# Optimization experiments

Hardware: AMD Instinct MI355X
Metric: run time of the kernel (lower is better)

Reference implementation:

```python
import jax, jax.numpy as jnp
import numpy as np

NUM_AREAS = 4
NUM_TICKS = 4
AREA_N = 2048          # neurons per area
N = NUM_AREAS * AREA_N # total neurons = 8192
D_IN = 1024
N_CLASSES = 1024
BATCH = 512
THRESHOLD = 0.05


def setup_inputs() -> dict:
    key = jax.random.key(0)
    ks = jax.random.split(key, 9)
    x = jax.random.normal(ks[0], (BATCH, D_IN), jnp.float32)
    Rw = jax.random.normal(ks[1], (NUM_AREAS, AREA_N, D_IN), jnp.float32) * 0.02
    rb = jax.random.normal(ks[2], (NUM_AREAS, AREA_N), jnp.float32) * 0.02
    W_blocks = jax.random.normal(ks[3], (NUM_AREAS, NUM_AREAS, AREA_N, AREA_N), jnp.float32) * 0.02
    # bias only on diagonal blocks (in_area == out_area), else zeros, as in torch code
    b_full = jax.random.normal(ks[4], (NUM_AREAS, AREA_N), jnp.float32) * 0.02
    b_blocks = jnp.zeros((NUM_AREAS, NUM_AREAS, AREA_N), jnp.float32)
    b_blocks = b_blocks.at[jnp.arange(NUM_AREAS), jnp.arange(NUM_AREAS)].set(b_full)
    # mask init: 0.5 on diagonal blocks, 0.05 off-diagonal
    eye = jnp.eye(NUM_AREAS, dtype=jnp.float32)
    mask = (0.05 + 0.45 * eye)[:, :, None, None] * jnp.ones((NUM_AREAS, NUM_AREAS, AREA_N, AREA_N), jnp.float32)
    Ow = jax.random.normal(ks[5], (N_CLASSES, N), jnp.float32) * 0.02
    Ob = jax.random.normal(ks[6], (N_CLASSES,), jnp.float32) * 0.02
    # KMeans-like neuron partition: random permutation split into equal areas
    area_idx = jax.random.permutation(ks[7], N).reshape(NUM_AREAS, AREA_N).astype(jnp.int64)
    return {"x": x, "Rw": Rw, "rb": rb, "W_blocks": W_blocks, "b_blocks": b_blocks,
            "mask": mask, "Ow": Ow, "Ob": Ob, "area_idx": area_idx}


def reference(x, Rw, rb, W_blocks, b_blocks, mask, Ow, Ob, area_idx):
    # Initial per-area encoding: Z[a] = tanh(x @ Rw[a].T + rb[a]) -> [A, B, n]
    Z = jnp.tanh(jnp.einsum('bd,and->abn', x, Rw) + rb[:, None, :])
    history = [Z]
    # Effective masked weights (clamp mask to [0,1])
    Weff = W_blocks * jnp.clip(mask, 0.0, 1.0)  # [A_out, A_in, n_out, n_in]
    for _ in range(NUM_TICKS):
        # data-dependent skip: connection fires only if mean|Z_in| > threshold
        gate = (jnp.mean(jnp.abs(Z), axis=(1, 2)) > THRESHOLD).astype(Z.dtype)  # [A_in]
        Zg = Z * gate[:, None, None]
        Z_next = jnp.einsum('ibm,oinm->obn', Zg, Weff)
        Z_next = Z_next + jnp.einsum('i,oin->on', gate, b_blocks)[:, None, :]
        Z = jnp.tanh(Z_next)
        history.append(Z)
    B = x.shape[0]
    # Scatter per-area activations back to flat neuron order
    Zperm = jnp.transpose(Z, (1, 0, 2)).reshape(B, N)  # columns ordered as area_idx.reshape(-1)
    Z_flat = jnp.zeros((B, N), x.dtype).at[:, area_idx.reshape(-1)].set(Zperm)
    logits = Z_flat @ Ow.T + Ob
    return logits, jnp.stack(history)  # history: [T+1, A, B, n]
```

## Files before the change

### kernel.cpp

```cpp
#include <hip/hip_runtime.h>
#include <stdint.h>

typedef unsigned short u16;
typedef float floatx4 __attribute__((ext_vector_type(4)));
typedef __bf16 bf16x8 __attribute__((ext_vector_type(8)));
typedef float f32x4v __attribute__((ext_vector_type(4)));
typedef unsigned u32x4v __attribute__((ext_vector_type(4)));

#define NUM_AREAS 4
#define AN 2048
#define NTOT 8192
#define BATCH 512
#define DIN 1024
#define NCLS 1024
#define THRESHOLD 0.05f
#define BAN (BATCH * AN)

__device__ __forceinline__ u16 f2bf(float f) {
    union { float f; unsigned u; } v; v.f = f;
    unsigned r = v.u + 0x7fffu + ((v.u >> 16) & 1u);
    return (u16)(r >> 16);
}

__device__ __forceinline__ void load_lds16(const u16* g, u16* l) {
    __builtin_amdgcn_global_load_lds((const __attribute__((address_space(1))) void*)g,
                                     (__attribute__((address_space(3))) void*)l,
                                     16, 0, 0);
}

__device__ __forceinline__ void gemm_db(const u16* __restrict__ A, int lda,
                                        const u16* __restrict__ Bm, int ldb,
                                        int klen, u16* sA, u16* sB,
                                        floatx4 acc[4][4]) {
    const int tid = threadIdx.x;
    const int t8 = tid * 8;
    const int lane = tid & 63;
    const int quad = lane >> 4;
    const int l15 = lane & 15;
    const int wm = ((tid >> 7) & 1) * 64;
    const int wn = ((tid >> 6) & 1) * 64;
    const int r0 = t8 >> 5;
    const int kk = t8 & 31;
    const int nst = klen >> 5;

    auto stage = [&](int buf, int k0) {
        const int bo = buf << 12;
        load_lds16(A + (size_t)r0 * lda + (k0 + kk), sA + bo + t8);
        load_lds16(Bm + (size_t)r0 * ldb + (k0 + kk), sB + bo + t8);
        load_lds16(A + (size_t)(r0 + 64) * lda + (k0 + kk), sA + bo + 2048 + t8);
        load_lds16(Bm + (size_t)(r0 + 64) * ldb + (k0 + kk), sB + bo + 2048 + t8);
    };

    stage(0, 0);
    __syncthreads();
    int buf = 0;
    for (int t = 0; t < nst; ++t) {
        const int bo = buf << 12;
        bf16x8 av[4], bv[4];
#pragma unroll
        for (int i = 0; i < 4; ++i)
            av[i] = *(const bf16x8*)(sA + bo + (wm + i * 16 + l15) * 32 + quad * 8);
#pragma unroll
        for (int i = 0; i < 4; ++i)
            bv[i] = *(const bf16x8*)(sB + bo + (wn + i * 16 + l15) * 32 + quad * 8);
        if (t + 1 < nst) stage(buf ^ 1, (t + 1) << 5);
#pragma unroll
        for (int mt = 0; mt < 4; ++mt)
#pragma unroll
            for (int nt = 0; nt < 4; ++nt)
                acc[mt][nt] = __builtin_amdgcn_mfma_f32_16x16x32_bf16(av[mt], bv[nt], acc[mt][nt], 0, 0, 0);
        __syncthreads();
        buf ^= 1;
    }
}

__global__ void k_init(const float* __restrict__ Ob, float* __restrict__ out,
                       float* __restrict__ gacc) {
    const int i = blockIdx.x * 256 + threadIdx.x;
    if (i < BATCH * NCLS) out[i] = Ob[i & (NCLS - 1)];
    if (i < 32) gacc[i] = 0.f;
}

__global__ void k_cvt(const float* __restrict__ src, u16* __restrict__ dst, int n8) {
    const int i = blockIdx.x * 256 + threadIdx.x;
    if (i >= n8) return;
    const float4 x0 = ((const float4*)src)[2 * i];
    const float4 x1 = ((const float4*)src)[2 * i + 1];
    uint4 o;
    o.x = (unsigned)f2bf(x0.x) | ((unsigned)f2bf(x0.y) << 16);
    o.y = (unsigned)f2bf(x0.z) | ((unsigned)f2bf(x0.w) << 16);
    o.z = (unsigned)f2bf(x1.x) | ((unsigned)f2bf(x1.y) << 16);
    o.w = (unsigned)f2bf(x1.z) | ((unsigned)f2bf(x1.w) << 16);
    ((uint4*)dst)[i] = o;
}

__global__ void k_weff(const float* __restrict__ W, const float* __restrict__ mask,
                       u16* __restrict__ dst) {
    const int i = blockIdx.x * 256 + threadIdx.x;
    const f32x4v* wp = (const f32x4v*)W + (size_t)4 * i;
    const f32x4v* mp = (const f32x4v*)mask + (size_t)4 * i;
    f32x4v w0 = wp[0], w1 = wp[1], w2 = wp[2], w3 = wp[3];
    f32x4v m0 = mp[0], m1 = mp[1], m2 = mp[2], m3 = mp[3];
    asm volatile("" :: "v"(w0), "v"(w1), "v"(w2), "v"(w3),
                       "v"(m0), "v"(m1), "v"(m2), "v"(m3));
    #define CL(m) fminf(fmaxf((m), 0.f), 1.f)
    #define PK(wa, ma, wb, mb) ((unsigned)f2bf((wa) * CL(ma)) | ((unsigned)f2bf((wb) * CL(mb)) << 16))
    u32x4v o0, o1;
    o0[0] = PK(w0[0], m0[0], w0[1], m0[1]);
    o0[1] = PK(w0[2], m0[2], w0[3], m0[3]);
    o0[2] = PK(w1[0], m1[0], w1[1], m1[1]);
    o0[3] = PK(w1[2], m1[2], w1[3], m1[3]);
    o1[0] = PK(w2[0], m2[0], w2[1], m2[1]);
    o1[1] = PK(w2[2], m2[2], w2[3], m2[3]);
    o1[2] = PK(w3[0], m3[0], w3[1], m3[1]);
    o1[3] = PK(w3[2], m3[2], w3[3], m3[3]);
    #undef PK
    #undef CL
    u32x4v* dp = (u32x4v*)dst + (size_t)2 * i;
    dp[0] = o0;
    dp[1] = o1;
}

__global__ void k_enc(const u16* __restrict__ xbf, const u16* __restrict__ rwbf,
                      const float* __restrict__ rb, float* __restrict__ hist0,
                      u16* __restrict__ z0, float* __restrict__ gacc) {
    __shared__ __align__(16) u16 smemA[8192];
    __shared__ __align__(16) u16 smemB[8192];
    __shared__ float red[4];
    floatx4 acc[4][4] = {};
    const int mb = blockIdx.y, nb = blockIdx.x;
    gemm_db(xbf + (size_t)mb * 128 * DIN, DIN,
            rwbf + (size_t)nb * 128 * DIN, DIN, DIN, smemA, smemB, acc);
    const int tid = threadIdx.x, lane = tid & 63, quad = lane >> 4, l15 = lane & 15;
    const int wm = ((tid >> 7) & 1) * 64, wn = ((tid >> 6) & 1) * 64;
    const int cbase = nb * 128;
    const int area = cbase >> 11;
    float asum = 0.f;
#pragma unroll
    for (int nt = 0; nt < 4; ++nt) {
        const int col = cbase + wn + nt * 16 + l15;
        const int n = col & (AN - 1);
        const float bias = rb[col];
#pragma unroll
        for (int mt = 0; mt < 4; ++mt) {
#pragma unroll
            for (int r = 0; r < 4; ++r) {
                const int row = mb * 128 + wm + mt * 16 + quad * 4 + r;
                const float z = tanhf(acc[mt][nt][r] + bias);
                asum += fabsf(z);
                const size_t idx = (size_t)area * BAN + (size_t)row * AN + n;
                hist0[idx] = z;
                z0[idx] = f2bf(z);
            }
        }
    }
    for (int off = 32; off > 0; off >>= 1) asum += __shfl_down(asum, off, 64);
    if (lane == 0) red[tid >> 6] = asum;
    __syncthreads();
    if (tid == 0) atomicAdd(&gacc[area], red[0] + red[1] + red[2] + red[3]);
}

__global__ void k_tick_mm(const u16* __restrict__ zprev, const u16* __restrict__ weff,
                          const float* __restrict__ gin, float* __restrict__ zacc) {
    __shared__ __align__(16) u16 smemA[8192];
    __shared__ __align__(16) u16 smemB[8192];
    const int nb = blockIdx.x, mb = blockIdx.y, i = blockIdx.z;
    const float thr = THRESHOLD * (float)BAN;
    if (!(gin[i] > thr)) return;
    floatx4 acc[4][4] = {};
    const int cbase = nb * 128;
    const int o = cbase >> 11;
    const int nbase = cbase & (AN - 1);
    gemm_db(zprev + (size_t)i * BAN + (size_t)mb * 128 * AN, AN,
            weff + ((size_t)(o * 4 + i) * AN + nbase) * AN, AN, AN,
            smemA, smemB, acc);
    float* __restrict__ dst = zacc + ((size_t)i * 4 + o) * BAN;
    const int tid = threadIdx.x, lane = tid & 63, quad = lane >> 4, l15 = lane & 15;
    const int wm = ((tid >> 7) & 1) * 64, wn = ((tid >> 6) & 1) * 64;
#pragma unroll
    for (int nt = 0; nt < 4; ++nt) {
        const int n = nbase + wn + nt * 16 + l15;
#pragma unroll
        for (int mt = 0; mt < 4; ++mt) {
#pragma unroll
            for (int r = 0; r < 4; ++r) {
                const int row = mb * 128 + wm + mt * 16 + quad * 4 + r;
                dst[(size_t)row * AN + n] = acc[mt][nt][r];
            }
        }
    }
}

__global__ void k_tick_ep(const float* __restrict__ zacc, const float* __restrict__ bblk,
                          const float* __restrict__ gin, float* __restrict__ hist,
                          u16* __restrict__ zcur, float* __restrict__ gout) {
    __shared__ float red[4];
    const int tid = threadIdx.x;
    const int t8 = (blockIdx.x * 256 + tid) * 8;
    const int o = t8 >> 20;
    const int n = t8 & (AN - 1);
    const int io = t8 & (BAN - 1);
    const float thr = THRESHOLD * (float)BAN;
    float s[8] = {0.f, 0.f, 0.f, 0.f, 0.f, 0.f, 0.f, 0.f};
#pragma unroll
    for (int i = 0; i < 4; ++i) {
        if (!(gin[i] > thr)) continue;
        const float4* p = (const float4*)(zacc + ((size_t)i * 4 + o) * BAN + io);
        const float4 x0 = p[0], x1 = p[1];
        const float4* bb = (const float4*)(bblk + (size_t)(o * 4 + i) * AN + n);
        const float4 b0 = bb[0], b1 = bb[1];
        s[0] += x0.x + b0.x; s[1] += x0.y + b0.y; s[2] += x0.z + b0.z; s[3] += x0.w + b0.w;
        s[4] += x1.x + b1.x; s[5] += x1.y + b1.y; s[6] += x1.z + b1.z; s[7] += x1.w + b1.w;
    }
    float4 h0, h1;
    uint4 zb;
    const float z0 = tanhf(s[0]), z1 = tanhf(s[1]), z2 = tanhf(s[2]), z3 = tanhf(s[3]);
    const float z4 = tanhf(s[4]), z5 = tanhf(s[5]), z6 = tanhf(s[6]), z7 = tanhf(s[7]);
    float asum = fabsf(z0) + fabsf(z1) + fabsf(z2) + fabsf(z3)
               + fabsf(z4) + fabsf(z5) + fabsf(z6) + fabsf(z7);
    h0.x = z0; h0.y = z1; h0.z = z2; h0.w = z3;
    h1.x = z4; h1.y = z5; h1.z = z6; h1.w = z7;
    zb.x = (unsigned)f2bf(z0) | ((unsigned)f2bf(z1) << 16);
    zb.y = (unsigned)f2bf(z2) | ((unsigned)f2bf(z3) << 16);
    zb.z = (unsigned)f2bf(z4) | ((unsigned)f2bf(z5) << 16);
    zb.w = (unsigned)f2bf(z6) | ((unsigned)f2bf(z7) << 16);
    ((float4*)(hist + t8))[0] = h0;
    ((float4*)(hist + t8))[1] = h1;
    *((uint4*)(zcur + t8)) = zb;
    for (int off = 32; off > 0; off >>= 1) asum += __shfl_down(asum, off, 64);
    if ((tid & 63) == 0) red[tid >> 6] = asum;
    __syncthreads();
    if (tid == 0) atomicAdd(&gout[o], red[0] + red[1] + red[2] + red[3]);
}

__global__ void k_scatter(const u16* __restrict__ z4, const int* __restrict__ aidx,
                          u16* __restrict__ zflat) {
    const int i = blockIdx.x * 256 + threadIdx.x;
    const int n = i & (AN - 1);
    const int bb = (i >> 11) & (BATCH - 1);
    const int a = i >> 20;
    const int j = aidx[a * AN + n];
    zflat[(size_t)bb * NTOT + j] = z4[i];
}

__global__ void k_out(const u16* __restrict__ zflat, const u16* __restrict__ owbf,
                      float* __restrict__ out) {
    __shared__ __align__(16) u16 smemA[8192];
    __shared__ __align__(16) u16 smemB[8192];
    floatx4 acc[4][4] = {};
    const int nb = blockIdx.x, mb = blockIdx.y, ks = blockIdx.z;
    gemm_db(zflat + (size_t)mb * 128 * NTOT + ks * 1024, NTOT,
            owbf + (size_t)nb * 128 * NTOT + ks * 1024, NTOT, 1024,
            smemA, smemB, acc);
    const int tid = threadIdx.x, lane = tid & 63, quad = lane >> 4, l15 = lane & 15;
    const int wm = ((tid >> 7) & 1) * 64, wn = ((tid >> 6) & 1) * 64;
#pragma unroll
    for (int mt = 0; mt < 4; ++mt)
#pragma unroll
        for (int nt = 0; nt < 4; ++nt)
#pragma unroll
            for (int r = 0; r < 4; ++r) {
                const int row = mb * 128 + wm + mt * 16 + quad * 4 + r;
                const int col = nb * 128 + wn + nt * 16 + l15;
                atomicAdd(&out[(size_t)row * NCLS + col], acc[mt][nt][r]);
            }
}

extern "C" void kernel_launch(void* const* d_in, const int* in_sizes, int n_in,
                              void* d_out, int out_size, void* d_ws, size_t ws_size,
                              hipStream_t stream) {
    (void)in_sizes; (void)n_in; (void)out_size; (void)ws_size;
    const float* x    = (const float*)d_in[0];
    const float* Rw   = (const float*)d_in[1];
    const float* rb   = (const float*)d_in[2];
    const float* Wb   = (const float*)d_in[3];
    const float* bblk = (const float*)d_in[4];
    const float* mask = (const float*)d_in[5];
    const float* Ow   = (const float*)d_in[6];
    const float* Ob   = (const float*)d_in[7];
    const int*   aidx = (const int*)d_in[8];

    float* out  = (float*)d_out;
    float* hist = out + (size_t)BATCH * NCLS;

    char* ws = (char*)d_ws;
    size_t off = 0;
    auto alloc = [&](size_t bytes) -> char* {
        char* p = ws + off;
        off += (bytes + 255) & ~(size_t)255;
        return p;
    };
    u16* weffbf = (u16*)alloc((size_t)16 * AN * AN * 2);
    float* zacc = (float*)alloc((size_t)16 * BAN * 4);
    u16* rwbf  = (u16*)zacc;
    u16* owbf  = (u16*)((char*)zacc + ((size_t)16 << 20));
    u16* zflat = (u16*)((char*)zacc + ((size_t)32 << 20));
    u16* xbf    = (u16*)alloc((size_t)BATCH * DIN * 2);
    u16* zb0    = (u16*)alloc((size_t)NUM_AREAS * BAN * 2);
    u16* zb1    = (u16*)alloc((size_t)NUM_AREAS * BAN * 2);
    float* gacc = (float*)alloc(32 * 4);
    u16* zb[2]  = { zb0, zb1 };

    k_init<<<(BATCH * NCLS + 255) / 256, 256, 0, stream>>>(Ob, out, gacc);
    k_cvt<<<(BATCH * DIN / 8) / 256, 256, 0, stream>>>(x, xbf, BATCH * DIN / 8);
    k_cvt<<<(NTOT * DIN / 8) / 256, 256, 0, stream>>>(Rw, rwbf, NTOT * DIN / 8);
    k_weff<<<16384, 256, 0, stream>>>(Wb, mask, weffbf);

    dim3 g1(64, 4);
    k_enc<<<g1, 256, 0, stream>>>(xbf, rwbf, rb, hist, zb[0], gacc);
    dim3 gmm(64, 4, 4);
    for (int t = 1; t <= 4; ++t) {
        k_tick_mm<<<gmm, 256, 0, stream>>>(zb[(t + 1) & 1], weffbf,
                                           gacc + (t - 1) * 4, zacc);
        k_tick_ep<<<2048, 256, 0, stream>>>(zacc, bblk, gacc + (t - 1) * 4,
                                            hist + (size_t)t * NUM_AREAS * BAN,
                                            zb[t & 1], gacc + t * 4);
    }
    k_cvt<<<(NCLS * NTOT / 8) / 256, 256, 0, stream>>>(Ow, owbf, NCLS * NTOT / 8);
    k_scatter<<<(NUM_AREAS * BAN) / 256, 256, 0, stream>>>(zb[0], aidx, zflat);
    k_out<<<dim3(8, 4, 8), 256, 0, stream>>>(zflat, owbf, out);
}
```

Before: 1.102 ms.

## Enlarge tick GEMM tiles to 256x256 with 8 waves and triple-buffered LDS

Rewrites the per-tick masked-weight GEMM to use 256x256 output tiles per block with 512 threads, each wave computing a 128x64 sub-tile, and a three-slot LDS ring that keeps two K-stages of loads in flight. Larger tiles raise arithmetic intensity and cut global traffic for the reused Z and Weff operands. The grid shrinks from 1024 to 256 blocks, which lowers parallelism on a large-CU GPU. Each thread also now holds 128 accumulator floats, which raises register pressure and may cap occupancy.

```diff
diff --git a/kernel.cpp b/kernel.cpp
--- a/kernel.cpp
+++ b/kernel.cpp
@@ -160,31 +160,87 @@
     if (tid == 0) atomicAdd(&gacc[area], red[0] + red[1] + red[2] + red[3]);
 }
 
-__global__ void k_tick_mm(const u16* __restrict__ zprev, const u16* __restrict__ weff,
-                          const float* __restrict__ gin, float* __restrict__ zacc) {
-    __shared__ __align__(16) u16 smemA[8192];
-    __shared__ __align__(16) u16 smemB[8192];
+__global__ __launch_bounds__(512, 2)
+void k_tick_mm(const u16* __restrict__ zprev, const u16* __restrict__ weff,
+               const float* __restrict__ gin, float* __restrict__ zacc) {
+    __shared__ __align__(16) u16 sA[3][8192];
+    __shared__ __align__(16) u16 sB[3][8192];
     const int nb = blockIdx.x, mb = blockIdx.y, i = blockIdx.z;
     const float thr = THRESHOLD * (float)BAN;
     if (!(gin[i] > thr)) return;
-    floatx4 acc[4][4] = {};
-    const int cbase = nb * 128;
-    const int o = cbase >> 11;
-    const int nbase = cbase & (AN - 1);
-    gemm_db(zprev + (size_t)i * BAN + (size_t)mb * 128 * AN, AN,
-            weff + ((size_t)(o * 4 + i) * AN + nbase) * AN, AN, AN,
-            smemA, smemB, acc);
+
+    const int o = nb >> 3;
+    const int nbase = (nb & 7) * 256;
+    const int tid = threadIdx.x;
+    const int lane = tid & 63, quad = lane >> 4, l15 = lane & 15;
+    const int w = tid >> 6;
+    const int wm = (w >> 2) * 128;
+    const int wn = (w & 3) * 64;
+
+    const u16* Abase = zprev + (size_t)i * BAN + (size_t)mb * 256 * AN;
+    const u16* Bbase = weff + ((size_t)(o * 4 + i) * AN + nbase) * AN;
+    const int r0 = tid >> 2;
+    const int kq = (tid & 3) * 8;
+    const u16* pA0 = Abase + (size_t)r0 * AN + kq;
+    const u16* pA1 = Abase + (size_t)(r0 + 128) * AN + kq;
+    const u16* pB0 = Bbase + (size_t)r0 * AN + kq;
+    const u16* pB1 = Bbase + (size_t)(r0 + 128) * AN + kq;
+    u16* dA0 = &sA[0][tid * 8];
+    u16* dA1 = &sA[0][tid * 8 + 4096];
+    u16* dB0 = &sB[0][tid * 8];
+    u16* dB1 = &sB[0][tid * 8 + 4096];
+
+    auto stage = [&](int slot, int kt) {
+        const int ko = kt * 32;
+        const int so = slot * 8192;
+        load_lds16(pA0 + ko, dA0 + so);
+        load_lds16(pA1 + ko, dA1 + so);
+        load_lds16(pB0 + ko, dB0 + so);
+        load_lds16(pB1 + ko, dB1 + so);
+    };
+
+    floatx4 acc[8][4] = {};
+
+    stage(0, 0);
+    stage(1, 1);
+    asm volatile("s_waitcnt vmcnt(4)" ::: "memory");
+    __builtin_amdgcn_s_barrier();
+
+    const int NKT = AN / 32;
+    for (int kt = 0; kt < NKT; ++kt) {
+        if (kt + 2 < NKT) stage((kt + 2) % 3, kt + 2);
+        const int sl = kt % 3;
+        bf16x8 av[8], bv[4];
+#pragma unroll
+        for (int mt = 0; mt < 8; ++mt)
+            av[mt] = *(const bf16x8*)(&sA[sl][(wm + mt * 16 + l15) * 32 + quad * 8]);
+#pragma unroll
+        for (int nt = 0; nt < 4; ++nt)
+            bv[nt] = *(const bf16x8*)(&sB[sl][(wn + nt * 16 + l15) * 32 + quad * 8]);
+        __builtin_amdgcn_s_setprio(1);
+#pragma unroll
+        for (int mt = 0; mt < 8; ++mt)
+#pragma unroll
+            for (int nt = 0; nt < 4; ++nt)
+                acc[mt][nt] = __builtin_amdgcn_mfma_f32_16x16x32_bf16(av[mt], bv[nt], acc[mt][nt], 0, 0, 0);
+        __builtin_amdgcn_s_setprio(0);
+        if (kt < NKT - 2) {
+            asm volatile("s_waitcnt vmcnt(4)" ::: "memory");
+        } else {
+            asm volatile("s_waitcnt vmcnt(0)" ::: "memory");
+        }
+        __builtin_amdgcn_s_barrier();
+    }
+
     float* __restrict__ dst = zacc + ((size_t)i * 4 + o) * BAN;
-    const int tid = threadIdx.x, lane = tid & 63, quad = lane >> 4, l15 = lane & 15;
-    const int wm = ((tid >> 7) & 1) * 64, wn = ((tid >> 6) & 1) * 64;
-#pragma unroll
-    for (int nt = 0; nt < 4; ++nt) {
-        const int n = nbase + wn + nt * 16 + l15;
-#pragma unroll
-        for (int mt = 0; mt < 4; ++mt) {
+#pragma unroll
+    for (int mt = 0; mt < 8; ++mt) {
+#pragma unroll
+        for (int nt = 0; nt < 4; ++nt) {
+            const int n = nbase + wn + nt * 16 + l15;
 #pragma unroll
             for (int r = 0; r < 4; ++r) {
-                const int row = mb * 128 + wm + mt * 16 + quad * 4 + r;
+                const int row = mb * 256 + wm + mt * 16 + quad * 4 + r;
                 dst[(size_t)row * AN + n] = acc[mt][nt][r];
             }
         }
@@ -308,9 +364,9 @@
 
     dim3 g1(64, 4);
     k_enc<<<g1, 256, 0, stream>>>(xbf, rwbf, rb, hist, zb[0], gacc);
-    dim3 gmm(64, 4, 4);
+    dim3 gmm(32, 2, 4);
     for (int t = 1; t <= 4; ++t) {
-        k_tick_mm<<<gmm, 256, 0, stream>>>(zb[(t + 1) & 1], weffbf,
+        k_tick_mm<<<gmm, 512, 0, stream>>>(zb[(t + 1) & 1], weffbf,
                                            gacc + (t - 1) * 4, zacc);
         k_tick_ep<<<2048, 256, 0, stream>>>(zacc, bblk, gacc + (t - 1) * 4,
                                             hist + (size_t)t * NUM_AREAS * BAN,
```

Result: slower. 1.128 ms (+2.3%).
